# Kernel tuning notes

Measured on AMD Instinct MI355X. Metric: run time of the kernel, lower is better.

The kernel has to match this reference:

```python
import jax, jax.numpy as jnp
import numpy as np
from jax import lax

B, T, F, H, NSTEPS = 512, 512, 64, 128, 8
HALF = H // 2
LN_EPS = 1e-5


def gru_cell(x, h, w_ih, w_hh, b_ih, b_hh):
    # PyTorch GRUCell math. x: (B, in), h: (B, H)
    gx = x @ w_ih.T + b_ih            # (B, 3H)
    gh = h @ w_hh.T + b_hh            # (B, 3H)
    rx, zx, nx = jnp.split(gx, 3, axis=-1)
    rh, zh, nh = jnp.split(gh, 3, axis=-1)
    r = jax.nn.sigmoid(rx + rh)
    z = jax.nn.sigmoid(zx + zh)
    n = jnp.tanh(nx + r * nh)
    return (1.0 - z) * n + z * h


def run_gru_layer(xs, h0, w_ih, w_hh, b_ih, b_hh):
    # xs: (T, B, in) -> (T, B, H), last hidden (B, H)
    def step(h, x_t):
        h = gru_cell(x_t, h, w_ih, w_hh, b_ih, b_hh)
        return h, h
    h_last, ys = lax.scan(step, h0, xs)
    return ys, h_last


def setup_inputs() -> dict:
    key = jax.random.key(0)
    ks = iter(jax.random.split(key, 64))
    s = 1.0 / np.sqrt(H)

    def p(shape):
        return jax.random.uniform(next(ks), shape, jnp.float32, -s, s)

    inp = {"x": jax.random.normal(next(ks), (B, T, F), jnp.float32)}
    # encoder: 3 GRU layers (layer 0 takes F features, layers 1-2 take H)
    for l, d_in in enumerate([F, H, H]):
        inp[f"e{l}w_ih"] = p((3 * H, d_in))
        inp[f"e{l}w_hh"] = p((3 * H, H))
        inp[f"e{l}b_ih"] = p((3 * H,))
        inp[f"e{l}b_hh"] = p((3 * H,))
    # additive (Bahdanau) attention
    inp["aWq"] = p((H, H)); inp["abq"] = p((H,))
    inp["aWk"] = p((H, H)); inp["abk"] = p((H,))
    inp["av"] = p((H,))
    # decoder GRU: input is cat([context, state]) -> 2H
    inp["dw_ih"] = p((3 * H, 2 * H)); inp["dw_hh"] = p((3 * H, H))
    inp["db_ih"] = p((3 * H,)); inp["db_hh"] = p((3 * H,))
    # head: LayerNorm -> Linear(H, H/2) -> ReLU -> Linear(H/2, 1)
    inp["lng"] = jnp.ones((H,), jnp.float32); inp["lnb"] = jnp.zeros((H,), jnp.float32)
    inp["w1"] = p((HALF, H)); inp["b1"] = p((HALF,))
    inp["w2"] = p((1, HALF)); inp["b2"] = p((1,))
    return inp


def reference(x,
              e0w_ih, e0w_hh, e0b_ih, e0b_hh,
              e1w_ih, e1w_hh, e1b_ih, e1b_hh,
              e2w_ih, e2w_hh, e2b_ih, e2b_hh,
              aWq, abq, aWk, abk, av,
              dw_ih, dw_hh, db_ih, db_hh,
              lng, lnb, w1, b1, w2, b2):
    b = x.shape[0]
    xs = jnp.transpose(x, (1, 0, 2))  # (T, B, F)
    h0 = jnp.zeros((b, H), x.dtype)
    # 3-layer encoder GRU (dropout is eval-mode no-op)
    ys, _ = run_gru_layer(xs, h0, e0w_ih, e0w_hh, e0b_ih, e0b_hh)
    ys, _ = run_gru_layer(ys, h0, e1w_ih, e1w_hh, e1b_ih, e1b_hh)
    ys, h_n = run_gru_layer(ys, h0, e2w_ih, e2w_hh, e2b_ih, e2b_hh)
    enc = jnp.transpose(ys, (1, 0, 2))  # (B, T, H)

    keys = enc @ aWk.T + abk  # precompute key projection once: (B, T, H)

    def dec_step(h, _):
        q = h @ aWq.T + abq                                   # (B, H)
        scores = jnp.einsum('bth,h->bt', jnp.tanh(keys + q[:, None, :]), av)
        w = jax.nn.softmax(scores, axis=-1)                   # (B, T)
        ctx = jnp.einsum('bt,bth->bh', w, enc)                # (B, H)
        h_new = gru_cell(jnp.concatenate([ctx, h], axis=-1), h,
                         dw_ih, dw_hh, db_ih, db_hh)
        mu = h_new.mean(-1, keepdims=True)
        var = ((h_new - mu) ** 2).mean(-1, keepdims=True)
        y = (h_new - mu) / jnp.sqrt(var + LN_EPS) * lng + lnb
        y = jax.nn.relu(y @ w1.T + b1)
        pred = y @ w2.T + b2                                  # (B, 1)
        return h_new, pred

    _, preds = lax.scan(dec_step, h_n, None, length=NSTEPS)   # (n_steps, B, 1)
    return jnp.transpose(preds, (1, 0, 2))                    # (B, n_steps, 1)
```

## Files before the change

### kernel.cpp

```cpp
#include <hip/hip_runtime.h>
#include <hip/hip_bf16.h>
#include <cstdint>
#include <cstddef>

#define T_LEN 512
#define B_SZ  512
#define F_IN  64
#define H_DIM 128
#define NSTEP 8

typedef __attribute__((ext_vector_type(8))) short short8;
typedef __attribute__((ext_vector_type(4))) float f32x4;

__device__ __forceinline__ float fsig(float x) { return 1.0f / (1.0f + __expf(-x)); }
__device__ __forceinline__ float ftanh(float x) {
  float e = __expf(-2.0f * fabsf(x));
  float t = (1.0f - e) / (1.0f + e);
  return copysignf(t, x);
}
__device__ __forceinline__ unsigned short bf16hi(float x) {
  __hip_bfloat16 h = __float2bfloat16(x);
  return *(unsigned short*)&h;
}
__device__ __forceinline__ float bf2f(unsigned short u) {
  return __uint_as_float(((unsigned)u) << 16);
}
__device__ __forceinline__ float bflo(unsigned u) { return __uint_as_float(u << 16); }
__device__ __forceinline__ float bfhi(unsigned u) { return __uint_as_float(u & 0xffff0000u); }

__device__ __forceinline__ void step_barrier() {
  asm volatile("s_waitcnt lgkmcnt(0)" ::: "memory");
  __builtin_amdgcn_s_barrier();
  asm volatile("" ::: "memory");
}

template <int CTRL>
__device__ __forceinline__ float dpp_add(float v) {
  int p = __builtin_amdgcn_update_dpp(0, __float_as_int(v), CTRL, 0xF, 0xF, true);
  return v + __int_as_float(p);
}
__device__ __forceinline__ float row_sum16(float v) {
  v = dpp_add<0xB1>(v);
  v = dpp_add<0x4E>(v);
  v = dpp_add<0x124>(v);
  v = dpp_add<0x128>(v);
  return v;
}

__device__ __forceinline__ void split8(const float* p, short8& hi, short8& lo) {
  #pragma unroll
  for (int i = 0; i < 8; ++i) {
    const float v = p[i];
    const unsigned short h = bf16hi(v);
    hi[i] = (short)h;
    lo[i] = (short)bf16hi(v - bf2f(h));
  }
}

__device__ __forceinline__ void split_f4pair(const float4 a, const float4 b,
                                             short8& hi, short8& lo) {
  const float v[8] = {a.x, a.y, a.z, a.w, b.x, b.y, b.z, b.w};
  #pragma unroll
  for (int j = 0; j < 8; ++j) {
    const unsigned short h = bf16hi(v[j]);
    hi[j] = (short)h;
    lo[j] = (short)bf16hi(v[j] - bf2f(h));
  }
}

__global__ __launch_bounds__(256) void prep_split(
    const float* __restrict__ w0, const float* __restrict__ w1,
    const float* __restrict__ w2,
    unsigned short* __restrict__ hi, unsigned short* __restrict__ lo)
{
  const int i = blockIdx.x * 256 + threadIdx.x;
  if (i >= 122880) return;
  float v = (i < 24576) ? w0[i] : ((i < 73728) ? w1[i - 24576] : w2[i - 73728]);
  const unsigned short h = bf16hi(v);
  hi[i] = h;
  lo[i] = bf16hi(v - bf2f(h));
}

template <int IS_L0>
__global__ __launch_bounds__(512, 2) void rec_fused(
    const float* x,
    const unsigned short* Xhi,
    const unsigned short* Xlo,
    const unsigned short* __restrict__ Wih_hi,
    const unsigned short* __restrict__ Wih_lo,
    const float* __restrict__ w_hh, const float* __restrict__ b_ih,
    const float* __restrict__ b_hh,
    unsigned short* Hhi, unsigned short* Hlo)
{
  constexpr int KD   = IS_L0 ? 64 : 128;
  constexpr int NCK  = KD / 32;
  constexpr int WROW = KD * 2;
  constexpr int WGRAN = WROW / 16;
  constexpr int XBUF = IS_L0 ? 4096 : 8192;

  __shared__ unsigned short Wlds[384 * KD];
  __shared__ float gxlds[8 * 2 * 384];
  __shared__ unsigned short hbh[2][2048], hbl[2][2048];
  __shared__ unsigned short hs[2][512];
  __shared__ __align__(16) unsigned char Xraw[2][XBUF];

  const int tid  = threadIdx.x;
  const int wv   = tid >> 6, lane = tid & 63;
  const int quad = lane >> 4, l16 = lane & 15;
  const int b0   = blockIdx.x * 2;
  const int c    = wv * 16 + l16;

  const f32x4 z4 = (f32x4){0.f, 0.f, 0.f, 0.f};

  {
    unsigned char* wb = (unsigned char*)Wlds;
    #pragma unroll
    for (int k = 0; k < (384 * WGRAN) / 512; ++k) {
      const int idx = k * 512 + tid;
      const int row = idx / WGRAN;
      const int gg  = idx % WGRAN;
      const uint4 v = *(const uint4*)&Wih_hi[(size_t)row * KD + gg * 8];
      *(uint4*)&wb[row * WROW + ((gg ^ (row & (WGRAN - 1))) * 16)] = v;
    }
  }

  short8 Wl_[3][NCK];
  #pragma unroll
  for (int g_ = 0; g_ < 3; ++g_)
    #pragma unroll
    for (int ck = 0; ck < NCK; ++ck)
      Wl_[g_][ck] = *(const short8*)&Wih_lo[(size_t)(g_ * 128 + c) * KD + ck * 32 + quad * 8];

  short8 Bh[3][4], Bl[3][4];
  #pragma unroll
  for (int g_ = 0; g_ < 3; ++g_)
    #pragma unroll
    for (int ck = 0; ck < 4; ++ck)
      split8(&w_hh[(size_t)(g_ * 128 + c) * 128 + ck * 32 + quad * 8],
             Bh[g_][ck], Bl[g_][ck]);

  float bias_r = 0.f, bias_z = 0.f, bihn = 0.f, bhhn = 0.f, h0 = 0.f, h1 = 0.f;
  if (quad == 0) {
    bias_r = b_ih[c] + b_hh[c];
    bias_z = b_ih[c + 128] + b_hh[c + 128];
    bihn = b_ih[c + 256];
    bhhn = b_hh[c + 256];
    hs[0][c] = 0; hs[0][128 + c] = 0;
    hs[0][256 + c] = 0; hs[0][384 + c] = 0;
  }

  const int t8 = tid & 255;
  const int sr = t8 >> 4;
  const int sg = tid & 15;
  uint4 xr = {0, 0, 0, 0};

  auto load_xr = [&](int tgn) {
    if constexpr (IS_L0) {
      if (tid < 256)
        xr = *(const uint4*)&x[((size_t)(b0 + (sr & 1)) * T_LEN + tgn + (sr >> 1)) * 64 + sg * 4];
    } else {
      const unsigned short* src = (tid < 256) ? Xhi : Xlo;
      xr = *(const uint4*)&src[((size_t)(tgn + (sr >> 1)) * B_SZ + b0 + (sr & 1)) * 128 + sg * 8];
    }
  };
  auto store_xr = [&](int buf) {
    unsigned char* dstb = &Xraw[buf][0];
    const int off = sr * 256 + ((sg ^ (sr & 7)) * 16);
    if constexpr (IS_L0) {
      if (tid < 256) *(uint4*)&dstb[off] = xr;
    } else {
      *(uint4*)&dstb[(tid < 256 ? 0 : 4096) + off] = xr;
    }
  };
  auto flush_h = [&](int buf, int tp) {
    const int ft = t8 >> 5, fr = (t8 >> 4) & 1, fs = t8 & 15;
    const size_t go = ((size_t)(tp + ft) * B_SZ + b0 + fr) * 128 + fs * 8;
    const int lo_ = (ft * 2 + fr) * 128 + fs * 8;
    if (tid < 256) *(uint4*)&Hhi[go] = *(const uint4*)&hbh[buf][lo_];
    else           *(uint4*)&Hlo[go] = *(const uint4*)&hbl[buf][lo_];
  };

  load_xr(0);
  store_xr(0);
  load_xr(8);
  __syncthreads();

  for (int g = 0; g < 64; ++g) {
    if (g > 0) flush_h((g - 1) & 1, g * 8 - 8);

    short8 Xhf[NCK], Xlf[NCK];
    {
      const unsigned char* xbuf = &Xraw[g & 1][0];
      if constexpr (IS_L0) {
        #pragma unroll
        for (int ck = 0; ck < 2; ++ck) {
          const int g0 = ck * 8 + quad * 2;
          const float4 f0 = *(const float4*)&xbuf[l16 * 256 + ((g0 ^ (l16 & 7)) * 16)];
          const float4 f1 = *(const float4*)&xbuf[l16 * 256 + (((g0 + 1) ^ (l16 & 7)) * 16)];
          split_f4pair(f0, f1, Xhf[ck], Xlf[ck]);
        }
      } else {
        #pragma unroll
        for (int ck = 0; ck < 4; ++ck) {
          const int go = ((ck * 4 + quad) ^ (l16 & 7)) * 16;
          Xhf[ck] = *(const short8*)&xbuf[l16 * 256 + go];
          Xlf[ck] = *(const short8*)&xbuf[4096 + l16 * 256 + go];
        }
      }
    }
    {
      f32x4 ax[3][2];
      const unsigned char* wb = (const unsigned char*)Wlds;
      #pragma unroll
      for (int g_ = 0; g_ < 3; ++g_) {
        ax[g_][0] = z4;
        ax[g_][1] = z4;
      }
      #pragma unroll
      for (int ck = 0; ck < NCK; ++ck) {
        const int p = (NCK == 4) ? (ck >> 1) : ck;
        #pragma unroll
        for (int g_ = 0; g_ < 3; ++g_) {
          const int n = g_ * 128 + c;
          const short8 wh = *(const short8*)&wb[n * WROW + (((ck * 4 + quad) ^ (n & (WGRAN - 1))) * 16)];
          ax[g_][p] = __builtin_amdgcn_mfma_f32_16x16x32_bf16(Xhf[ck], wh, ax[g_][p], 0, 0, 0);
          ax[g_][p] = __builtin_amdgcn_mfma_f32_16x16x32_bf16(Xhf[ck], Wl_[g_][ck], ax[g_][p], 0, 0, 0);
          ax[g_][p] = __builtin_amdgcn_mfma_f32_16x16x32_bf16(Xlf[ck], wh, ax[g_][p], 0, 0, 0);
        }
      }
      #pragma unroll
      for (int g_ = 0; g_ < 3; ++g_)
        #pragma unroll
        for (int reg = 0; reg < 4; ++reg) {
          const int tt_ = quad * 2 + (reg >> 1);
          const int r_  = reg & 1;
          gxlds[(tt_ * 2 + r_) * 384 + g_ * 128 + c] = ax[g_][0][reg] + ax[g_][1][reg];
        }
    }
    step_barrier();

    #pragma unroll
    for (int tt = 0; tt < 8; ++tt) {
      float gr0 = 0.f, gz0 = 0.f, gn0v = 0.f, gr1 = 0.f, gz1 = 0.f, gn1v = 0.f;
      if (quad == 0) {
        const float* gp = &gxlds[tt * 768 + c];
        gr0 = gp[0];   gz0 = gp[128]; gn0v = gp[256];
        gr1 = gp[384]; gz1 = gp[512]; gn1v = gp[640];
      }

      short8 Af[4];
      #pragma unroll
      for (int ck = 0; ck < 4; ++ck) {
        const int ad = (l16 & 3) * 128 + ck * 32 + quad * 8;
        Af[ck] = *(const short8*)&hs[tt & 1][ad];
      }

      f32x4 acc[3][2];
      #pragma unroll
      for (int g_ = 0; g_ < 3; ++g_) {
        #pragma unroll
        for (int p = 0; p < 2; ++p) {
          const int k0 = p * 2;
          acc[g_][p] = __builtin_amdgcn_mfma_f32_16x16x32_bf16(Af[k0], Bh[g_][k0], z4, 0, 0, 0);
          acc[g_][p] = __builtin_amdgcn_mfma_f32_16x16x32_bf16(Af[k0], Bl[g_][k0], acc[g_][p], 0, 0, 0);
          acc[g_][p] = __builtin_amdgcn_mfma_f32_16x16x32_bf16(Af[k0 + 1], Bh[g_][k0 + 1], acc[g_][p], 0, 0, 0);
          acc[g_][p] = __builtin_amdgcn_mfma_f32_16x16x32_bf16(Af[k0 + 1], Bl[g_][k0 + 1], acc[g_][p], 0, 0, 0);
        }
      }

      if (quad == 0) {
        const float ghr0 = acc[0][0][0] + acc[0][0][2] + acc[0][1][0] + acc[0][1][2];
        const float ghr1 = acc[0][0][1] + acc[0][0][3] + acc[0][1][1] + acc[0][1][3];
        const float ghz0 = acc[1][0][0] + acc[1][0][2] + acc[1][1][0] + acc[1][1][2];
        const float ghz1 = acc[1][0][1] + acc[1][0][3] + acc[1][1][1] + acc[1][1][3];
        const float ghn0 = acc[2][0][0] + acc[2][0][2] + acc[2][1][0] + acc[2][1][2];
        const float ghn1 = acc[2][0][1] + acc[2][0][3] + acc[2][1][1] + acc[2][1][3];
        const float r0 = fsig(gr0 + ghr0 + bias_r);
        const float z0 = fsig(gz0 + ghz0 + bias_z);
        const float nv0 = ftanh(gn0v + bihn + r0 * (ghn0 + bhhn));
        const float hn0 = (1.0f - z0) * nv0 + z0 * h0;
        const float r1 = fsig(gr1 + ghr1 + bias_r);
        const float z1 = fsig(gz1 + ghz1 + bias_z);
        const float nv1 = ftanh(gn1v + bihn + r1 * (ghn1 + bhhn));
        const float hn1 = (1.0f - z1) * nv1 + z1 * h1;
        h0 = hn0; h1 = hn1;
        const int nb = (tt + 1) & 1;
        const unsigned short hh0 = bf16hi(hn0), hh1 = bf16hi(hn1);
        const unsigned short hl0 = bf16hi(hn0 - bf2f(hh0));
        const unsigned short hl1 = bf16hi(hn1 - bf2f(hh1));
        hs[nb][c] = hh0;         hs[nb][128 + c] = hh1;
        hs[nb][256 + c] = hl0;   hs[nb][384 + c] = hl1;
        const int hb = (tt * 2) * 128 + c;
        hbh[g & 1][hb] = hh0;       hbh[g & 1][hb + 128] = hh1;
        hbl[g & 1][hb] = hl0;       hbl[g & 1][hb + 128] = hl1;
      }

      if (tt == 7 && g + 1 < 64) {
        store_xr((g + 1) & 1);
        if (g + 2 < 64) load_xr((g + 2) * 8);
      }
      step_barrier();
    }
  }
  flush_h(1, 504);
}

__global__ __launch_bounds__(256) void keys_gemm(
    const unsigned short* __restrict__ Ahi, const unsigned short* __restrict__ Alo,
    const float* __restrict__ aWk, const float* __restrict__ abk,
    unsigned short* __restrict__ Kbt)
{
  __shared__ unsigned short Ah[64 * 40], Al[64 * 40];
  __shared__ unsigned short Bh[128 * 136], Bl[128 * 136];
  const int tid  = threadIdx.x;
  const int wave = tid >> 6, lane = tid & 63;
  const int quad = lane >> 4, l16 = lane & 15;
  const size_t m0 = (size_t)blockIdx.x * 64;

  for (int i = tid; i < 16384; i += 256) {
    const float v = aWk[i];
    const unsigned short h = bf16hi(v);
    const int r = i >> 7, k = i & 127;
    Bh[r * 136 + k] = h;
    Bl[r * 136 + k] = bf16hi(v - bf2f(h));
  }

  f32x4 acc[8];
  #pragma unroll
  for (int i = 0; i < 8; ++i) acc[i] = (f32x4){0.f, 0.f, 0.f, 0.f};
  float bias[8];
  #pragma unroll
  for (int nt = 0; nt < 8; ++nt) bias[nt] = abk[nt * 16 + l16];

  const int r = tid >> 2, c8 = (tid & 3) * 8;
  for (int kc = 0; kc < 128; kc += 32) {
    __syncthreads();
    const size_t src = (m0 + r) * 128 + kc + c8;
    *(uint4*)&Ah[r * 40 + c8] = *(const uint4*)&Ahi[src];
    *(uint4*)&Al[r * 40 + c8] = *(const uint4*)&Alo[src];
    __syncthreads();
    const short8 a_hi = *(const short8*)&Ah[(wave * 16 + l16) * 40 + quad * 8];
    const short8 a_lo = *(const short8*)&Al[(wave * 16 + l16) * 40 + quad * 8];
    #pragma unroll
    for (int nt = 0; nt < 8; ++nt) {
      const short8 b_hi = *(const short8*)&Bh[(nt * 16 + l16) * 136 + kc + quad * 8];
      const short8 b_lo = *(const short8*)&Bl[(nt * 16 + l16) * 136 + kc + quad * 8];
      acc[nt] = __builtin_amdgcn_mfma_f32_16x16x32_bf16(a_hi, b_hi, acc[nt], 0, 0, 0);
      acc[nt] = __builtin_amdgcn_mfma_f32_16x16x32_bf16(a_hi, b_lo, acc[nt], 0, 0, 0);
      acc[nt] = __builtin_amdgcn_mfma_f32_16x16x32_bf16(a_lo, b_hi, acc[nt], 0, 0, 0);
    }
  }
  #pragma unroll
  for (int nt = 0; nt < 8; ++nt) {
    #pragma unroll
    for (int reg = 0; reg < 4; ++reg) {
      const size_t m = m0 + wave * 16 + quad * 4 + reg;
      const size_t b = m & 511, t = m >> 9;
      const int n = nt * 16 + l16;
      Kbt[(b * T_LEN + t) * 128 + n] = bf16hi(acc[nt][reg] + bias[nt]);
    }
  }
}

__global__ __launch_bounds__(512) void save_lasth(
    const unsigned short* __restrict__ Hhi, const unsigned short* __restrict__ Hlo,
    float* __restrict__ lastH)
{
  const int i = blockIdx.x * 512 + threadIdx.x;
  const size_t src = ((size_t)(T_LEN - 1) * B_SZ) * 128 + i;
  lastH[i] = bf2f(Hhi[src]) + bf2f(Hlo[src]);
}

__global__ __launch_bounds__(256) void transpose_h(
    const unsigned short* __restrict__ Hhi, unsigned short* __restrict__ Hbt)
{
  const int b  = blockIdx.x >> 3;
  const int tg = blockIdx.x & 7;
  #pragma unroll
  for (int j = 0; j < 4; ++j) {
    const int id = threadIdx.x * 4 + j;
    const int tl = id >> 4;
    const int ch = (id & 15) * 8;
    const int t  = tg * 64 + tl;
    const uint4 v = *(const uint4*)&Hhi[((size_t)t * B_SZ + b) * 128 + ch];
    *(uint4*)&Hbt[((size_t)b * T_LEN + t) * 128 + ch] = v;
  }
}

__global__ __launch_bounds__(512) void decoder(
    const unsigned short* __restrict__ Hbt,
    const unsigned short* __restrict__ Kbt,
    const float* __restrict__ lastH,
    const float* __restrict__ aWq, const float* __restrict__ abq,
    const float* __restrict__ av,
    const float* __restrict__ dwih, const float* __restrict__ dwhh,
    const float* __restrict__ dbih, const float* __restrict__ dbhh,
    const float* __restrict__ lng, const float* __restrict__ lnb,
    const float* __restrict__ w1, const float* __restrict__ b1,
    const float* __restrict__ w2, const float* __restrict__ b2,
    float* __restrict__ out)
{
  __shared__ float h_s[128], q_s[128], av_s[128], s_s[512], w_s[512];
  __shared__ float part[8][128], u_s[256], gx_s[384], gh_s[384], y_s[128];
  __shared__ float red[16];
  const int b = blockIdx.x, tid = threadIdx.x;
  const int wave = tid >> 6, lane = tid & 63;
  const int tslot = lane >> 4, ks = lane & 15;

  if (tid < 128) {
    h_s[tid] = lastH[(size_t)b * 128 + tid];
    av_s[tid] = av[tid];
  }
  __syncthreads();

  for (int step = 0; step < NSTEP; ++step) {
    if (tid < 128) {
      float acc = abq[tid];
      const float* wr = &aWq[(size_t)tid * 128];
      #pragma unroll 8
      for (int k4 = 0; k4 < 32; ++k4) {
        const float4 hv = *(const float4*)&h_s[k4 * 4];
        const float4 wv = *(const float4*)&wr[k4 * 4];
        acc += hv.x * wv.x + hv.y * wv.y + hv.z * wv.z + hv.w * wv.w;
      }
      q_s[tid] = acc;
    }
    __syncthreads();
    #pragma unroll 2
    for (int it = 0; it < 16; ++it) {
      const int t = it * 32 + wave * 4 + tslot;
      const size_t kb = ((size_t)b * T_LEN + t) * 128 + ks * 8;
      const uint4 uh = *(const uint4*)&Kbt[kb];
      const float4 q0 = *(const float4*)&q_s[ks * 8];
      const float4 q1 = *(const float4*)&q_s[ks * 8 + 4];
      const float4 a0 = *(const float4*)&av_s[ks * 8];
      const float4 a1 = *(const float4*)&av_s[ks * 8 + 4];
      float acc = ftanh(bflo(uh.x) + q0.x) * a0.x + ftanh(bfhi(uh.x) + q0.y) * a0.y
                + ftanh(bflo(uh.y) + q0.z) * a0.z + ftanh(bfhi(uh.y) + q0.w) * a0.w
                + ftanh(bflo(uh.z) + q1.x) * a1.x + ftanh(bfhi(uh.z) + q1.y) * a1.y
                + ftanh(bflo(uh.w) + q1.z) * a1.z + ftanh(bfhi(uh.w) + q1.w) * a1.w;
      acc = row_sum16(acc);
      if (ks == 0) s_s[t] = acc;
    }
    __syncthreads();
    {
      const float sv = s_s[tid];
      float mx = sv;
      #pragma unroll
      for (int o = 32; o; o >>= 1) mx = fmaxf(mx, __shfl_xor(mx, o, 64));
      if (lane == 0) red[wave] = mx;
      __syncthreads();
      mx = red[0];
      #pragma unroll
      for (int i = 1; i < 8; ++i) mx = fmaxf(mx, red[i]);
      const float e = __expf(sv - mx);
      float sm = e;
      #pragma unroll
      for (int o = 32; o; o >>= 1) sm += __shfl_xor(sm, o, 64);
      if (lane == 0) red[8 + wave] = sm;
      __syncthreads();
      float tot = red[8];
      #pragma unroll
      for (int i = 1; i < 8; ++i) tot += red[8 + i];
      w_s[tid] = e / tot;
    }
    __syncthreads();
    {
      const int th = tid >> 6;
      const int c2 = (tid & 63) * 2;
      float acc0 = 0.0f, acc1 = 0.0f;
      #pragma unroll 4
      for (int q = 0; q < 64; ++q) {
        const int t = th * 64 + q;
        const unsigned u = *(const unsigned*)&Hbt[((size_t)b * T_LEN + t) * 128 + c2];
        const float wt = w_s[t];
        acc0 += wt * bflo(u);
        acc1 += wt * bfhi(u);
      }
      part[th][c2] = acc0;
      part[th][c2 + 1] = acc1;
    }
    __syncthreads();
    if (tid < 128) {
      float s = part[0][tid];
      #pragma unroll
      for (int i = 1; i < 8; ++i) s += part[i][tid];
      u_s[tid] = s;
      u_s[128 + tid] = h_s[tid];
    }
    __syncthreads();
    if (tid < 384) {
      const int j = tid;
      float gxv = dbih[j], ghv = dbhh[j];
      const float* wxr = &dwih[(size_t)j * 256];
      const float* whr = &dwhh[(size_t)j * 128];
      #pragma unroll 8
      for (int k4 = 0; k4 < 64; ++k4) {
        const float4 uv = *(const float4*)&u_s[k4 * 4];
        const float4 wv = *(const float4*)&wxr[k4 * 4];
        gxv += uv.x * wv.x + uv.y * wv.y + uv.z * wv.z + uv.w * wv.w;
      }
      #pragma unroll 8
      for (int k4 = 0; k4 < 32; ++k4) {
        const float4 hv = *(const float4*)&h_s[k4 * 4];
        const float4 wv = *(const float4*)&whr[k4 * 4];
        ghv += hv.x * wv.x + hv.y * wv.y + hv.z * wv.z + hv.w * wv.w;
      }
      gx_s[j] = gxv; gh_s[j] = ghv;
    }
    __syncthreads();
    if (tid < 128) {
      const float r = fsig(gx_s[tid] + gh_s[tid]);
      const float z = fsig(gx_s[128 + tid] + gh_s[128 + tid]);
      const float n = ftanh(gx_s[256 + tid] + r * gh_s[256 + tid]);
      const float hn = (1.0f - z) * n + z * h_s[tid];
      h_s[tid] = hn;
      float s1 = hn, s2 = hn * hn;
      #pragma unroll
      for (int o = 32; o; o >>= 1) { s1 += __shfl_xor(s1, o, 64); s2 += __shfl_xor(s2, o, 64); }
      if ((tid & 63) == 0) { red[tid >> 6] = s1; red[4 + (tid >> 6)] = s2; }
    }
    __syncthreads();
    if (tid < 128) {
      const float hn  = h_s[tid];
      const float mu  = (red[0] + red[1]) * (1.0f / 128.0f);
      const float var = (red[4] + red[5]) * (1.0f / 128.0f) - mu * mu;
      y_s[tid] = (hn - mu) / sqrtf(var + 1e-5f) * lng[tid] + lnb[tid];
    }
    __syncthreads();
    if (tid < 64) {
      float acc = b1[tid];
      const float* wr = &w1[(size_t)tid * 128];
      #pragma unroll 8
      for (int k4 = 0; k4 < 32; ++k4) {
        const float4 yv = *(const float4*)&y_s[k4 * 4];
        const float4 wv = *(const float4*)&wr[k4 * 4];
        acc += yv.x * wv.x + yv.y * wv.y + yv.z * wv.z + yv.w * wv.w;
      }
      acc = fmaxf(acc, 0.0f);
      float v = acc * w2[tid];
      #pragma unroll
      for (int o = 32; o; o >>= 1) v += __shfl_xor(v, o, 64);
      if (tid == 0) out[(size_t)b * NSTEP + step] = v + b2[0];
    }
    __syncthreads();
  }
}

extern "C" void kernel_launch(void* const* d_in, const int* in_sizes, int n_in,
                              void* d_out, int out_size, void* d_ws, size_t ws_size,
                              hipStream_t stream)
{
  (void)in_sizes; (void)n_in; (void)out_size; (void)ws_size;
  const float* x    = (const float*)d_in[0];
  const float* ewih[3] = {(const float*)d_in[1], (const float*)d_in[5], (const float*)d_in[9]};
  const float* ewhh[3] = {(const float*)d_in[2], (const float*)d_in[6], (const float*)d_in[10]};
  const float* ebih[3] = {(const float*)d_in[3], (const float*)d_in[7], (const float*)d_in[11]};
  const float* ebhh[3] = {(const float*)d_in[4], (const float*)d_in[8], (const float*)d_in[12]};
  const float* aWq  = (const float*)d_in[13];
  const float* abq  = (const float*)d_in[14];
  const float* aWk  = (const float*)d_in[15];
  const float* abk  = (const float*)d_in[16];
  const float* av   = (const float*)d_in[17];
  const float* dwih = (const float*)d_in[18];
  const float* dwhh = (const float*)d_in[19];
  const float* dbih = (const float*)d_in[20];
  const float* dbhh = (const float*)d_in[21];
  const float* lng  = (const float*)d_in[22];
  const float* lnb  = (const float*)d_in[23];
  const float* w1   = (const float*)d_in[24];
  const float* b1   = (const float*)d_in[25];
  const float* w2   = (const float*)d_in[26];
  const float* b2   = (const float*)d_in[27];

  const size_t HN = (size_t)T_LEN * B_SZ * H_DIM;
  unsigned short* Hhi = (unsigned short*)d_ws;
  unsigned short* Hlo = Hhi + HN;
  float* regionC = (float*)(Hlo + HN);
  unsigned short* Whi = (unsigned short*)(regionC + 25165824 + 65536);
  unsigned short* Wlo = Whi + 122880;
  unsigned short* Kbt = (unsigned short*)regionC;
  float* lastH = regionC + 16777216;

  prep_split<<<dim3(480), dim3(256), 0, stream>>>(ewih[0], ewih[1], ewih[2], Whi, Wlo);

  rec_fused<1><<<dim3(256), dim3(512), 0, stream>>>(
      x, nullptr, nullptr, Whi, Wlo,
      ewhh[0], ebih[0], ebhh[0], Hhi, Hlo);
  rec_fused<0><<<dim3(256), dim3(512), 0, stream>>>(
      nullptr, Hhi, Hlo, Whi + 24576, Wlo + 24576,
      ewhh[1], ebih[1], ebhh[1], Hhi, Hlo);
  rec_fused<0><<<dim3(256), dim3(512), 0, stream>>>(
      nullptr, Hhi, Hlo, Whi + 73728, Wlo + 73728,
      ewhh[2], ebih[2], ebhh[2], Hhi, Hlo);

  keys_gemm<<<dim3(4096), dim3(256), 0, stream>>>(Hhi, Hlo, aWk, abk, Kbt);
  save_lasth<<<dim3(128), dim3(512), 0, stream>>>(Hhi, Hlo, lastH);
  transpose_h<<<dim3(4096), dim3(256), 0, stream>>>(Hhi, Hlo);
  decoder<<<dim3(512), dim3(512), 0, stream>>>(
      Hlo, Kbt, lastH, aWq, abq, av, dwih, dwhh, dbih, dbhh,
      lng, lnb, w1, b1, w2, b2, (float*)d_out);
}
```

Before: 2.389 ms.

## Load input fragments straight to registers and spread GRU gate epilogue across quads

Removes the LDS staging buffer for input tiles. Each lane now loads its MFMA A-fragment directly from global memory into registers and prefetches the next chunk after the input-projection MFMAs. The gate pre-activations are stored interleaved with the biases folded in, so one float4 read per row replaces scattered scalar reads. The hidden state is written in a rotated layout so that all four quads compute the gates redundantly and each writes one hi/lo element, instead of only quad 0 doing four stores. This adds redundant transcendental work and more live registers for the prefetched inputs.

```diff
diff --git a/kernel.cpp b/kernel.cpp
--- a/kernel.cpp
+++ b/kernel.cpp
@@ -96,13 +96,11 @@
   constexpr int NCK  = KD / 32;
   constexpr int WROW = KD * 2;
   constexpr int WGRAN = WROW / 16;
-  constexpr int XBUF = IS_L0 ? 4096 : 8192;
 
   __shared__ unsigned short Wlds[384 * KD];
-  __shared__ float gxlds[8 * 2 * 384];
+  __shared__ float gxldsF[8 * 1040];
   __shared__ unsigned short hbh[2][2048], hbl[2][2048];
   __shared__ unsigned short hs[2][512];
-  __shared__ __align__(16) unsigned char Xraw[2][XBUF];
 
   const int tid  = threadIdx.x;
   const int wv   = tid >> 6, lane = tid & 63;
@@ -139,39 +137,41 @@
       split8(&w_hh[(size_t)(g_ * 128 + c) * 128 + ck * 32 + quad * 8],
              Bh[g_][ck], Bl[g_][ck]);
 
-  float bias_r = 0.f, bias_z = 0.f, bihn = 0.f, bhhn = 0.f, h0 = 0.f, h1 = 0.f;
-  if (quad == 0) {
-    bias_r = b_ih[c] + b_hh[c];
-    bias_z = b_ih[c + 128] + b_hh[c + 128];
-    bihn = b_ih[c + 256];
-    bhhn = b_hh[c + 256];
-    hs[0][c] = 0; hs[0][128 + c] = 0;
-    hs[0][256 + c] = 0; hs[0][384 + c] = 0;
-  }
+  const float bias_r = b_ih[c] + b_hh[c];
+  const float bias_z = b_ih[c + 128] + b_hh[c + 128];
+  const float bihn   = b_ih[c + 256];
+  const float bhhn   = b_hh[c + 256];
+  float h0 = 0.f, h1 = 0.f;
+  hs[0][tid & 511] = 0;
+
+  const int arow = l16 & 3;
+  const int K0   = arow * 32 + (((quad + arow) & 3) * 8);
+  const int hswr = ((c >> 5) * 128) + quad * 32
+                 + (((((c >> 3) & 3) + quad) & 3) * 8) + (c & 7);
+
+  uint4  xh[4], xl[4];
+  float4 xf[4];
+  auto load_x = [&](int tgn) {
+    if constexpr (IS_L0) {
+      #pragma unroll
+      for (int ck = 0; ck < 2; ++ck) {
+        const size_t base =
+            ((size_t)(b0 + (l16 & 1)) * T_LEN + tgn + (l16 >> 1)) * 64 + ck * 32 + quad * 8;
+        xf[ck * 2]     = *(const float4*)&x[base];
+        xf[ck * 2 + 1] = *(const float4*)&x[base + 4];
+      }
+    } else {
+      #pragma unroll
+      for (int ck = 0; ck < 4; ++ck) {
+        const size_t base =
+            ((size_t)(tgn + (l16 >> 1)) * B_SZ + b0 + (l16 & 1)) * 128 + ck * 32 + quad * 8;
+        xh[ck] = *(const uint4*)&Xhi[base];
+        xl[ck] = *(const uint4*)&Xlo[base];
+      }
+    }
+  };
 
   const int t8 = tid & 255;
-  const int sr = t8 >> 4;
-  const int sg = tid & 15;
-  uint4 xr = {0, 0, 0, 0};
-
-  auto load_xr = [&](int tgn) {
-    if constexpr (IS_L0) {
-      if (tid < 256)
-        xr = *(const uint4*)&x[((size_t)(b0 + (sr & 1)) * T_LEN + tgn + (sr >> 1)) * 64 + sg * 4];
-    } else {
-      const unsigned short* src = (tid < 256) ? Xhi : Xlo;
-      xr = *(const uint4*)&src[((size_t)(tgn + (sr >> 1)) * B_SZ + b0 + (sr & 1)) * 128 + sg * 8];
-    }
-  };
-  auto store_xr = [&](int buf) {
-    unsigned char* dstb = &Xraw[buf][0];
-    const int off = sr * 256 + ((sg ^ (sr & 7)) * 16);
-    if constexpr (IS_L0) {
-      if (tid < 256) *(uint4*)&dstb[off] = xr;
-    } else {
-      *(uint4*)&dstb[(tid < 256 ? 0 : 4096) + off] = xr;
-    }
-  };
   auto flush_h = [&](int buf, int tp) {
     const int ft = t8 >> 5, fr = (t8 >> 4) & 1, fs = t8 & 15;
     const size_t go = ((size_t)(tp + ft) * B_SZ + b0 + fr) * 128 + fs * 8;
@@ -180,42 +180,22 @@
     else           *(uint4*)&Hlo[go] = *(const uint4*)&hbl[buf][lo_];
   };
 
-  load_xr(0);
-  store_xr(0);
-  load_xr(8);
+  load_x(0);
   __syncthreads();
 
   for (int g = 0; g < 64; ++g) {
     if (g > 0) flush_h((g - 1) & 1, g * 8 - 8);
 
-    short8 Xhf[NCK], Xlf[NCK];
-    {
-      const unsigned char* xbuf = &Xraw[g & 1][0];
-      if constexpr (IS_L0) {
-        #pragma unroll
-        for (int ck = 0; ck < 2; ++ck) {
-          const int g0 = ck * 8 + quad * 2;
-          const float4 f0 = *(const float4*)&xbuf[l16 * 256 + ((g0 ^ (l16 & 7)) * 16)];
-          const float4 f1 = *(const float4*)&xbuf[l16 * 256 + (((g0 + 1) ^ (l16 & 7)) * 16)];
-          split_f4pair(f0, f1, Xhf[ck], Xlf[ck]);
-        }
-      } else {
-        #pragma unroll
-        for (int ck = 0; ck < 4; ++ck) {
-          const int go = ((ck * 4 + quad) ^ (l16 & 7)) * 16;
-          Xhf[ck] = *(const short8*)&xbuf[l16 * 256 + go];
-          Xlf[ck] = *(const short8*)&xbuf[4096 + l16 * 256 + go];
-        }
-      }
+    short8 Xhf[2], Xlf[2];
+    if constexpr (IS_L0) {
+      split_f4pair(xf[0], xf[1], Xhf[0], Xlf[0]);
+      split_f4pair(xf[2], xf[3], Xhf[1], Xlf[1]);
     }
     {
       f32x4 ax[3][2];
       const unsigned char* wb = (const unsigned char*)Wlds;
       #pragma unroll
-      for (int g_ = 0; g_ < 3; ++g_) {
-        ax[g_][0] = z4;
-        ax[g_][1] = z4;
-      }
+      for (int g_ = 0; g_ < 3; ++g_) { ax[g_][0] = z4; ax[g_][1] = z4; }
       #pragma unroll
       for (int ck = 0; ck < NCK; ++ck) {
         const int p = (NCK == 4) ? (ck >> 1) : ck;
@@ -223,37 +203,38 @@
         for (int g_ = 0; g_ < 3; ++g_) {
           const int n = g_ * 128 + c;
           const short8 wh = *(const short8*)&wb[n * WROW + (((ck * 4 + quad) ^ (n & (WGRAN - 1))) * 16)];
-          ax[g_][p] = __builtin_amdgcn_mfma_f32_16x16x32_bf16(Xhf[ck], wh, ax[g_][p], 0, 0, 0);
-          ax[g_][p] = __builtin_amdgcn_mfma_f32_16x16x32_bf16(Xhf[ck], Wl_[g_][ck], ax[g_][p], 0, 0, 0);
-          ax[g_][p] = __builtin_amdgcn_mfma_f32_16x16x32_bf16(Xlf[ck], wh, ax[g_][p], 0, 0, 0);
+          short8 ah, al;
+          if constexpr (IS_L0) { ah = Xhf[ck]; al = Xlf[ck]; }
+          else { ah = *(const short8*)&xh[ck]; al = *(const short8*)&xl[ck]; }
+          ax[g_][p] = __builtin_amdgcn_mfma_f32_16x16x32_bf16(ah, wh, ax[g_][p], 0, 0, 0);
+          ax[g_][p] = __builtin_amdgcn_mfma_f32_16x16x32_bf16(ah, Wl_[g_][ck], ax[g_][p], 0, 0, 0);
+          ax[g_][p] = __builtin_amdgcn_mfma_f32_16x16x32_bf16(al, wh, ax[g_][p], 0, 0, 0);
         }
       }
-      #pragma unroll
-      for (int g_ = 0; g_ < 3; ++g_)
+      if (g + 1 < 64) load_x((g + 1) * 8);
+      #pragma unroll
+      for (int g_ = 0; g_ < 3; ++g_) {
+        const float bg = (g_ == 0) ? bias_r : (g_ == 1) ? bias_z : bihn;
         #pragma unroll
         for (int reg = 0; reg < 4; ++reg) {
           const int tt_ = quad * 2 + (reg >> 1);
           const int r_  = reg & 1;
-          gxlds[(tt_ * 2 + r_) * 384 + g_ * 128 + c] = ax[g_][0][reg] + ax[g_][1][reg];
+          gxldsF[tt_ * 1040 + r_ * 520 + c * 4 + g_] =
+              ax[g_][0][reg] + ax[g_][1][reg] + bg;
         }
+      }
     }
     step_barrier();
 
     #pragma unroll
     for (int tt = 0; tt < 8; ++tt) {
-      float gr0 = 0.f, gz0 = 0.f, gn0v = 0.f, gr1 = 0.f, gz1 = 0.f, gn1v = 0.f;
-      if (quad == 0) {
-        const float* gp = &gxlds[tt * 768 + c];
-        gr0 = gp[0];   gz0 = gp[128]; gn0v = gp[256];
-        gr1 = gp[384]; gz1 = gp[512]; gn1v = gp[640];
-      }
+      const float4 ga = *(const float4*)&gxldsF[tt * 1040 + c * 4];
+      const float4 gb = *(const float4*)&gxldsF[tt * 1040 + 520 + c * 4];
 
       short8 Af[4];
       #pragma unroll
-      for (int ck = 0; ck < 4; ++ck) {
-        const int ad = (l16 & 3) * 128 + ck * 32 + quad * 8;
-        Af[ck] = *(const short8*)&hs[tt & 1][ad];
-      }
+      for (int ck = 0; ck < 4; ++ck)
+        Af[ck] = *(const short8*)&hs[tt & 1][ck * 128 + K0];
 
       f32x4 acc[3][2];
       #pragma unroll
@@ -268,36 +249,37 @@
         }
       }
 
+      const float ghr0 = acc[0][0][0] + acc[0][0][2] + acc[0][1][0] + acc[0][1][2];
+      const float ghr1 = acc[0][0][1] + acc[0][0][3] + acc[0][1][1] + acc[0][1][3];
+      const float ghz0 = acc[1][0][0] + acc[1][0][2] + acc[1][1][0] + acc[1][1][2];
+      const float ghz1 = acc[1][0][1] + acc[1][0][3] + acc[1][1][1] + acc[1][1][3];
+      const float ghn0 = acc[2][0][0] + acc[2][0][2] + acc[2][1][0] + acc[2][1][2];
+      const float ghn1 = acc[2][0][1] + acc[2][0][3] + acc[2][1][1] + acc[2][1][3];
+      const float r0 = fsig(ga.x + ghr0);
+      const float z0 = fsig(ga.y + ghz0);
+      const float nv0 = ftanh(ga.z + r0 * (ghn0 + bhhn));
+      const float hn0 = (1.0f - z0) * nv0 + z0 * h0;
+      const float r1 = fsig(gb.x + ghr1);
+      const float z1 = fsig(gb.y + ghz1);
+      const float nv1 = ftanh(gb.z + r1 * (ghn1 + bhhn));
+      const float hn1 = (1.0f - z1) * nv1 + z1 * h1;
+      h0 = hn0; h1 = hn1;
+
+      const int nb = (tt + 1) & 1;
+      const float hnsel = (quad & 1) ? hn1 : hn0;
+      const unsigned short uh = bf16hi(hnsel);
+      unsigned short val = uh;
+      if (quad >= 2) val = bf16hi(hnsel - bf2f(uh));
+      hs[nb][hswr] = val;
+
       if (quad == 0) {
-        const float ghr0 = acc[0][0][0] + acc[0][0][2] + acc[0][1][0] + acc[0][1][2];
-        const float ghr1 = acc[0][0][1] + acc[0][0][3] + acc[0][1][1] + acc[0][1][3];
-        const float ghz0 = acc[1][0][0] + acc[1][0][2] + acc[1][1][0] + acc[1][1][2];
-        const float ghz1 = acc[1][0][1] + acc[1][0][3] + acc[1][1][1] + acc[1][1][3];
-        const float ghn0 = acc[2][0][0] + acc[2][0][2] + acc[2][1][0] + acc[2][1][2];
-        const float ghn1 = acc[2][0][1] + acc[2][0][3] + acc[2][1][1] + acc[2][1][3];
-        const float r0 = fsig(gr0 + ghr0 + bias_r);
-        const float z0 = fsig(gz0 + ghz0 + bias_z);
-        const float nv0 = ftanh(gn0v + bihn + r0 * (ghn0 + bhhn));
-        const float hn0 = (1.0f - z0) * nv0 + z0 * h0;
-        const float r1 = fsig(gr1 + ghr1 + bias_r);
-        const float z1 = fsig(gz1 + ghz1 + bias_z);
-        const float nv1 = ftanh(gn1v + bihn + r1 * (ghn1 + bhhn));
-        const float hn1 = (1.0f - z1) * nv1 + z1 * h1;
-        h0 = hn0; h1 = hn1;
-        const int nb = (tt + 1) & 1;
-        const unsigned short hh0 = bf16hi(hn0), hh1 = bf16hi(hn1);
+        const unsigned short hh0 = uh;
         const unsigned short hl0 = bf16hi(hn0 - bf2f(hh0));
+        const unsigned short hh1 = bf16hi(hn1);
         const unsigned short hl1 = bf16hi(hn1 - bf2f(hh1));
-        hs[nb][c] = hh0;         hs[nb][128 + c] = hh1;
-        hs[nb][256 + c] = hl0;   hs[nb][384 + c] = hl1;
         const int hb = (tt * 2) * 128 + c;
         hbh[g & 1][hb] = hh0;       hbh[g & 1][hb + 128] = hh1;
         hbl[g & 1][hb] = hl0;       hbl[g & 1][hb + 128] = hl1;
-      }
-
-      if (tt == 7 && g + 1 < 64) {
-        store_xr((g + 1) & 1);
-        if (g + 2 < 64) load_xr((g + 2) * 8);
       }
       step_barrier();
     }
```

After: 2.332 ms. 1.02x faster.
